# Kernel optimization log

Measured on AMD Instinct MI355X. Metric: run time of the kernel, lower is better.

The kernel has to match this reference:

```python
import jax, jax.numpy as jnp
import numpy as np

OUT = 3      # pooled output size (fmap_size//4 = 14//4 = 3)
RATIO = 2    # roi_align sampling ratio (fixed; torchvision adaptive ratio for 14/3 bins is 2)
P = 20       # num_persons


def _bilinear(fm, y, x):
    # fm: [C,H,W]; y,x broadcastable coordinate grids. torchvision aligned=False semantics.
    C, H, W = fm.shape
    y, x = jnp.broadcast_arrays(y, x)
    valid = (y > -1.0) & (y < H) & (x > -1.0) & (x < W)
    y = jnp.clip(y, 0.0, H - 1.0)
    x = jnp.clip(x, 0.0, W - 1.0)
    y0 = jnp.floor(y).astype(jnp.int32)
    x0 = jnp.floor(x).astype(jnp.int32)
    y1 = jnp.minimum(y0 + 1, H - 1)
    x1 = jnp.minimum(x0 + 1, W - 1)
    ly = y - y0
    lx = x - x0
    hy = 1.0 - ly
    hx = 1.0 - lx
    v00 = fm[:, y0, x0]
    v01 = fm[:, y0, x1]
    v10 = fm[:, y1, x0]
    v11 = fm[:, y1, x1]
    val = hy * hx * v00 + hy * lx * v01 + ly * hx * v10 + ly * lx * v11
    return jnp.where(valid, val, 0.0)  # [C, ...]


def _roi_align_one(fm, box):
    # fm: [C,H,W], box: [4] = (x1,y1,x2,y2) in feature-map coords -> [C,OUT,OUT]
    x1, y1, x2, y2 = box
    bw = (x2 - x1) / OUT
    bh = (y2 - y1) / OUT
    off = (jnp.arange(OUT * RATIO, dtype=fm.dtype) + 0.5) / RATIO  # bin-unit offsets
    xs = x1 + off * bw
    ys = y1 + off * bh
    vals = _bilinear(fm, ys[:, None], xs[None, :])  # [C, OUT*RATIO, OUT*RATIO]
    C = fm.shape[0]
    return vals.reshape(C, OUT, RATIO, OUT, RATIO).mean(axis=(2, 4))


def setup_inputs() -> dict:
    key = jax.random.key(0)
    ks = jax.random.split(key, 8)
    B, N, NB, C, FS = 128, 8, 27, 1024, 14
    fmap = jax.random.normal(ks[0], (B, C, FS, FS), jnp.float32)
    # boxes in feature-map coordinates with x1<x2, y1<y2
    lo = jax.random.uniform(ks[1], (B, N, 2), jnp.float32) * 10.0
    ext = 2.0 + jax.random.uniform(ks[2], (B, N, 2), jnp.float32) * 4.0
    hi = jnp.minimum(lo + ext, float(FS))
    boxes = jnp.concatenate([lo, hi], axis=-1)  # [B,N,4] (x1,y1,x2,y2)
    # unique person ids per frame (scatter target indices)
    pids = jax.vmap(lambda k: jax.random.permutation(k, P)[:N])(jax.random.split(ks[3], B)).astype(jnp.int32)
    w1 = jax.random.normal(ks[4], (512, C), jnp.float32) * 0.02
    w2 = jax.random.normal(ks[5], (256, 512), jnp.float32) * 0.05
    fc1_w = jax.random.normal(ks[6], (1024, 256 * OUT * OUT), jnp.float32) * 0.02
    fc1_b = jnp.zeros((1024,), jnp.float32)
    fc2_w = jax.random.normal(ks[7], (27, 1024), jnp.float32) * 0.02
    fc2_b = jnp.zeros((27,), jnp.float32)
    return {"fmap": fmap, "boxes": boxes, "pids": pids, "w1": w1, "w2": w2,
            "fc1_w": fc1_w, "fc1_b": fc1_b, "fc2_w": fc2_w, "fc2_b": fc2_b}


def _forward(fmap, boxes, pids, w1, w2, fc1_w, fc1_b, fc2_w, fc2_b):
    B, N = boxes.shape[:2]
    # per-image, per-box ROI align: [B,N,C,3,3]
    roi = jax.vmap(jax.vmap(_roi_align_one, in_axes=(None, 0)), in_axes=(0, 0))(fmap, boxes)
    # behavior_conv: two bias-free 1x1 convs (no nonlinearity between)
    h = jnp.einsum('bnchw,oc->bnohw', roi, w1)
    h = jnp.einsum('bnchw,oc->bnohw', h, w2)  # [B,N,256,3,3]
    feat = h.reshape(B, N, -1)                # [B,N,2304]
    bidx = jnp.broadcast_to(jnp.arange(B)[:, None], (B, N))
    # scatter into behavior_tensor keyed by person id (unique pids per frame -> well-defined)
    bt = jnp.zeros((B, P, feat.shape[-1]), feat.dtype).at[bidx, pids].set(feat)
    mean_b = bt.mean(axis=0)                  # [P,2304] mean over batch
    cur = bt[bidx, pids]                      # [B,N,2304]
    diff = mean_b[pids] - cur
    # behavior_fc (dropout is identity at inference)
    h1 = jax.nn.relu(jnp.einsum('bnd,hd->bnh', diff, fc1_w) + fc1_b)
    return jnp.einsum('bnh,oh->bno', h1, fc2_w) + fc2_b  # [B,N,num_behaviors]


def reference(fmap, boxes, pids, w1, w2, fc1_w, fc1_b, fc2_w, fc2_b):
    # fmap is detached and roi_align runs under no_grad in the original
    return _forward(jax.lax.stop_gradient(fmap), jax.lax.stop_gradient(boxes), pids,
                    w1, w2, fc1_w, fc1_b, fc2_w, fc2_b)
```

## Files before the change

kernel.cpp:

```cpp
#include <hip/hip_runtime.h>
#include <hip/hip_bf16.h>
#include <cstddef>
#include <cstdint>

#define B_   128
#define N_   8
#define C_   1024
#define FS_  14
#define POS_ 196
#define P_   20
#define HWC_ 9
#define ROWS_ 9216
#define CMID_ 256
#define FEATD_ 2304
#define H1_  1024
#define O_   27

typedef __attribute__((ext_vector_type(8))) short bf16x8;
typedef __attribute__((ext_vector_type(4))) float f32x4;

__device__ __forceinline__ void gld16(const void* g, void* l) {
    __builtin_amdgcn_global_load_lds(
        (const __attribute__((address_space(1))) unsigned int*)g,
        (__attribute__((address_space(3))) unsigned int*)l, 16, 0, 0);
}

__global__ __launch_bounds__(256) void wcombine_split_kernel(
    const float* __restrict__ w1,
    const float* __restrict__ w2,
    float* __restrict__ wpart)
{
    const int tid = threadIdx.x;
    const int tx = tid & 15, ty = tid >> 4;
    const int c0 = blockIdx.x * 64;
    const int o0 = blockIdx.y * 64;
    const int kb = blockIdx.z * 64;
    __shared__ __align__(16) float As[16][68];
    __shared__ __align__(16) float Bs[16][68];
    float acc[4][4] = {};
    for (int k0 = kb; k0 < kb + 64; k0 += 16) {
        for (int i = tid; i < 64 * 16; i += 256) {
            int k = i & 15, m = i >> 4;
            As[k][m] = w2[(size_t)(o0 + m) * 512 + k0 + k];
        }
        for (int i = tid; i < 64 * 16; i += 256) {
            int n = i & 63, k = i >> 6;
            Bs[k][n] = w1[(size_t)(k0 + k) * 1024 + c0 + n];
        }
        __syncthreads();
        #pragma unroll
        for (int k = 0; k < 16; ++k) {
            float4 a = *(const float4*)&As[k][ty * 4];
            float4 b = *(const float4*)&Bs[k][tx * 4];
            float av[4] = {a.x, a.y, a.z, a.w};
            float bv[4] = {b.x, b.y, b.z, b.w};
            #pragma unroll
            for (int i = 0; i < 4; ++i)
                #pragma unroll
                for (int j = 0; j < 4; ++j)
                    acc[i][j] += av[i] * bv[j];
        }
        __syncthreads();
    }
    float* dst = wpart + (size_t)blockIdx.z * (256 * 1024);
    for (int i = 0; i < 4; ++i) {
        float4 v = make_float4(acc[i][0], acc[i][1], acc[i][2], acc[i][3]);
        *(float4*)&dst[(size_t)(o0 + ty * 4 + i) * 1024 + c0 + tx * 4] = v;
    }
}

__global__ __launch_bounds__(256) void wc_reduce_kernel(
    const float* __restrict__ wpart, __hip_bfloat16* __restrict__ Wc)
{
    int idx = blockIdx.x * 256 + threadIdx.x;
    float s = 0.f;
    #pragma unroll
    for (int z = 0; z < 8; ++z) s += wpart[(size_t)z * (256 * 1024) + idx];
    Wc[idx] = __float2bfloat16(s);
}

__global__ __launch_bounds__(576) void roi_kernel(
    const float* __restrict__ fmap,
    const float* __restrict__ boxes,
    __hip_bfloat16* __restrict__ roi_mat)
{
    const int b = blockIdx.y;
    const int c0 = blockIdx.x * 64;
    const int tid = threadIdx.x;
    const int c_local = tid & 63;
    const int cell = tid >> 6;
    const int ch = cell / 3, cw = cell % 3;
    __shared__ float stage[64 * 197];

    const float* src = fmap + (size_t)(b * C_ + c0) * POS_;
    for (int i4 = tid; i4 < (64 * POS_) / 4; i4 += 576) {
        float4 v = ((const float4*)src)[i4];
        int base = i4 * 4;
        int c = base / POS_;
        int pos = base - c * POS_;
        float* dst = &stage[c * 197 + pos];
        dst[0] = v.x; dst[1] = v.y; dst[2] = v.z; dst[3] = v.w;
    }
    __syncthreads();

    const float* ch_ptr = &stage[c_local * 197];
    for (int n = 0; n < N_; ++n) {
        const float* bx = boxes + (size_t)(b * N_ + n) * 4;
        float x1 = bx[0], y1 = bx[1], x2 = bx[2], y2 = bx[3];
        float bw = (x2 - x1) * (1.0f / 3.0f);
        float bh = (y2 - y1) * (1.0f / 3.0f);
        float acc = 0.0f;
        #pragma unroll
        for (int si = 0; si < 2; ++si) {
            float yy = y1 + ((float)(2 * ch + si) + 0.5f) * 0.5f * bh;
            #pragma unroll
            for (int sj = 0; sj < 2; ++sj) {
                float xx = x1 + ((float)(2 * cw + sj) + 0.5f) * 0.5f * bw;
                bool valid = (yy > -1.0f) && (yy < (float)FS_) &&
                             (xx > -1.0f) && (xx < (float)FS_);
                float y = fminf(fmaxf(yy, 0.0f), (float)(FS_ - 1));
                float x = fminf(fmaxf(xx, 0.0f), (float)(FS_ - 1));
                int y0 = (int)floorf(y);
                int x0 = (int)floorf(x);
                int y1i = min(y0 + 1, FS_ - 1);
                int x1i = min(x0 + 1, FS_ - 1);
                float ly = y - (float)y0, lx = x - (float)x0;
                float hy = 1.0f - ly,     hx = 1.0f - lx;
                float v00 = ch_ptr[y0 * FS_ + x0];
                float v01 = ch_ptr[y0 * FS_ + x1i];
                float v10 = ch_ptr[y1i * FS_ + x0];
                float v11 = ch_ptr[y1i * FS_ + x1i];
                float val = hy * hx * v00 + hy * lx * v01 +
                            ly * hx * v10 + ly * lx * v11;
                acc += valid ? val : 0.0f;
            }
        }
        roi_mat[(size_t)((b * N_ + n) * HWC_ + cell) * C_ + c0 + c_local] =
            __float2bfloat16(acc * 0.25f);
    }
}

template<int EPI>
__global__ __launch_bounds__(256) void mfma_gemm_kernel(
    const __hip_bfloat16* __restrict__ A,
    const __hip_bfloat16* __restrict__ Bm,
    const float* __restrict__ bias,
    float* __restrict__ C, int K)
{
    const int tid = threadIdx.x;
    const int wave = tid >> 6, lane = tid & 63;
    const int r0 = blockIdx.y * 64, n0 = blockIdx.x * 64;
    const int wm = (wave >> 1) * 32, wn = (wave & 1) * 32;
    const int m16 = lane & 15, quad = lane >> 4;
    __shared__ __align__(16) __hip_bfloat16 As[64 * 64];
    __shared__ __align__(16) __hip_bfloat16 Bs[64 * 64];

    f32x4 acc[2][2];
    #pragma unroll
    for (int i = 0; i < 2; ++i)
        #pragma unroll
        for (int j = 0; j < 2; ++j)
            acc[i][j] = (f32x4){0.f, 0.f, 0.f, 0.f};

    const int s0 = wave * 64 + lane;
    const int ms0 = s0 >> 3, cs0 = (s0 & 7) ^ (ms0 & 7);
    const int s1 = 256 + s0;
    const int ms1 = s1 >> 3, cs1 = (s1 & 7) ^ (ms1 & 7);
    const size_t rA0 = (size_t)(r0 + ms0) * K + cs0 * 8;
    const size_t rA1 = (size_t)(r0 + ms1) * K + cs1 * 8;
    const size_t rB0 = (size_t)(n0 + ms0) * K + cs0 * 8;
    const size_t rB1 = (size_t)(n0 + ms1) * K + cs1 * 8;

    for (int k0 = 0; k0 < K; k0 += 64) {
        gld16(A + rA0 + k0, &As[wave * 512]);
        gld16(Bm + rB0 + k0, &Bs[wave * 512]);
        gld16(A + rA1 + k0, &As[2048 + wave * 512]);
        gld16(Bm + rB1 + k0, &Bs[2048 + wave * 512]);
        __syncthreads();
        #pragma unroll
        for (int ks = 0; ks < 2; ++ks) {
            bf16x8 af[2], bfv[2];
            #pragma unroll
            for (int t = 0; t < 2; ++t) {
                int m = wm + t * 16 + m16;
                int cp = (ks * 4 + quad) ^ (m & 7);
                af[t] = *(const bf16x8*)&As[(m * 8 + cp) * 8];
                int n = wn + t * 16 + m16;
                int cq = (ks * 4 + quad) ^ (n & 7);
                bfv[t] = *(const bf16x8*)&Bs[(n * 8 + cq) * 8];
            }
            #pragma unroll
            for (int i = 0; i < 2; ++i)
                #pragma unroll
                for (int j = 0; j < 2; ++j)
                    acc[i][j] = __builtin_amdgcn_mfma_f32_16x16x32_bf16(
                        af[i], bfv[j], acc[i][j], 0, 0, 0);
        }
        __syncthreads();
    }

    #pragma unroll
    for (int i = 0; i < 2; ++i) {
        #pragma unroll
        for (int j = 0; j < 2; ++j) {
            int col = n0 + wn + j * 16 + m16;
            int rbase = r0 + wm + i * 16 + quad * 4;
            if (EPI == 0) {
                #pragma unroll
                for (int g = 0; g < 4; ++g) {
                    int r = rbase + g;
                    int bn = r / 9, hw = r - bn * 9;
                    C[(size_t)bn * FEATD_ + hw * 256 + col] = acc[i][j][g];
                }
            } else {
                float bv = bias[col];
                #pragma unroll
                for (int g = 0; g < 4; ++g) {
                    int r = rbase + g;
                    float v = acc[i][j][g] + bv;
                    C[(size_t)r * H1_ + col] = v > 0.f ? v : 0.f;
                }
            }
        }
    }
}

__global__ __launch_bounds__(256) void fc1w_perm_kernel(
    const float* __restrict__ src, __hip_bfloat16* __restrict__ dst)
{
    int h = blockIdx.y;
    int d2 = blockIdx.x * 256 + threadIdx.x;
    int hw = d2 >> 8, o = d2 & 255;
    dst[(size_t)h * FEATD_ + d2] =
        __float2bfloat16(src[(size_t)h * FEATD_ + o * HWC_ + hw]);
}

__global__ __launch_bounds__(64) void invmap_kernel(
    const int* __restrict__ pids, int* __restrict__ inv)
{
    int b = blockIdx.x;
    int p = threadIdx.x;
    if (p < P_) {
        int v = -1;
        for (int n = 0; n < N_; ++n)
            if (pids[b * N_ + n] == p) v = n;
        inv[b * P_ + p] = v;
    }
}

__global__ __launch_bounds__(256) void meanb_kernel(
    const float* __restrict__ feat, const int* __restrict__ inv,
    float* __restrict__ mean_b)
{
    int p = blockIdx.x;
    int d = blockIdx.y * 256 + threadIdx.x;
    float acc = 0.0f;
    for (int b = 0; b < B_; ++b) {
        int n = inv[b * P_ + p];
        if (n >= 0) acc += feat[(size_t)(b * N_ + n) * FEATD_ + d];
    }
    mean_b[(size_t)p * FEATD_ + d] = acc * (1.0f / (float)B_);
}

__global__ __launch_bounds__(256) void diff_kernel(
    const float* __restrict__ feat, const float* __restrict__ mean_b,
    const int* __restrict__ pids, __hip_bfloat16* __restrict__ diff)
{
    int r = blockIdx.x;
    int pid = pids[r];
    const float* fr = feat + (size_t)r * FEATD_;
    const float* mr = mean_b + (size_t)pid * FEATD_;
    __hip_bfloat16* dr = diff + (size_t)r * FEATD_;
    for (int d = threadIdx.x; d < FEATD_; d += 256)
        dr[d] = __float2bfloat16(mr[d] - fr[d]);
}

__global__ __launch_bounds__(256) void fc2_kernel(
    const float* __restrict__ h1, const float* __restrict__ fc2_w,
    const float* __restrict__ fc2_b, float* __restrict__ out)
{
    int bn = blockIdx.x;
    int tid = threadIdx.x;
    __shared__ __align__(16) float row[H1_];
    __shared__ float partial[32][8];
    ((float4*)row)[tid] = ((const float4*)(h1 + (size_t)bn * H1_))[tid];
    __syncthreads();
    int o = tid >> 3, part = tid & 7;
    float acc = 0.0f;
    if (o < O_) {
        const float* wrow = fc2_w + (size_t)o * H1_ + part * 128;
        const float* hrow = row + part * 128;
        #pragma unroll 4
        for (int j = 0; j < 128; ++j) acc += hrow[j] * wrow[j];
    }
    partial[o][part] = acc;
    __syncthreads();
    if (part == 0 && o < O_) {
        float s = fc2_b[o];
        #pragma unroll
        for (int p = 0; p < 8; ++p) s += partial[o][p];
        out[(size_t)bn * O_ + o] = s;
    }
}

extern "C" void kernel_launch(void* const* d_in, const int* in_sizes, int n_in,
                              void* d_out, int out_size, void* d_ws, size_t ws_size,
                              hipStream_t stream) {
    const float* fmap  = (const float*)d_in[0];
    const float* boxes = (const float*)d_in[1];
    const int*   pids  = (const int*)  d_in[2];
    const float* w1    = (const float*)d_in[3];
    const float* w2    = (const float*)d_in[4];
    const float* fc1_w = (const float*)d_in[5];
    const float* fc1_b = (const float*)d_in[6];
    const float* fc2_w = (const float*)d_in[7];
    const float* fc2_b = (const float*)d_in[8];
    float* out = (float*)d_out;

    char* wsb = (char*)d_ws;
    __hip_bfloat16* Wc    = (__hip_bfloat16*)wsb;
    __hip_bfloat16* roi   = Wc + 256 * 1024;
    __hip_bfloat16* fc1wp = roi + (size_t)ROWS_ * C_;
    __hip_bfloat16* diffp = fc1wp + (size_t)H1_ * FEATD_;
    float* feat   = (float*)(diffp + (size_t)H1_ * FEATD_);
    float* mean_b = feat + (size_t)(B_ * N_) * FEATD_;
    float* h1     = mean_b + (size_t)P_ * FEATD_;
    int*   inv    = (int*)(h1 + (size_t)(B_ * N_) * H1_);
    float* wpart  = (float*)(inv + 128 * P_ + 64);

    hipLaunchKernelGGL(wcombine_split_kernel, dim3(16, 4, 8), dim3(256), 0, stream,
                       w1, w2, wpart);
    hipLaunchKernelGGL(wc_reduce_kernel, dim3(1024), dim3(256), 0, stream,
                       wpart, Wc);
    hipLaunchKernelGGL(roi_kernel, dim3(16, 128), dim3(576), 0, stream,
                       fmap, boxes, roi);
    hipLaunchKernelGGL(fc1w_perm_kernel, dim3(9, 1024), dim3(256), 0, stream,
                       fc1_w, fc1wp);
    hipLaunchKernelGGL((mfma_gemm_kernel<0>), dim3(4, 144), dim3(256), 0, stream,
                       roi, Wc, (const float*)nullptr, feat, 1024);
    hipLaunchKernelGGL(invmap_kernel, dim3(128), dim3(64), 0, stream,
                       pids, inv);
    hipLaunchKernelGGL(meanb_kernel, dim3(20, 9), dim3(256), 0, stream,
                       feat, inv, mean_b);
    hipLaunchKernelGGL(diff_kernel, dim3(1024), dim3(256), 0, stream,
                       feat, mean_b, pids, diffp);
    hipLaunchKernelGGL((mfma_gemm_kernel<1>), dim3(16, 16), dim3(256), 0, stream,
                       diffp, fc1wp, fc1_b, h1, FEATD_);
    hipLaunchKernelGGL(fc2_kernel, dim3(1024), dim3(256), 0, stream,
                       h1, fc2_w, fc2_b, out);
}
```

Measured before the change: 313.2 us.

## Apply channel-mixing GEMM before ROI align, on all feature-map positions

Since ROI align and the 1x1 convs are both linear, the combined weight is now applied to every fmap position (128*196 rows, K=1024, N=256) before ROI align. ROI align then samples the 256-channel bf16 result instead of 1024 fp32 channels and writes feat directly. This drops the 9216x1024 roi intermediate and cuts the bilinear work fourfold. In exchange the GEMM grows from 9216 to 25088 rows, and fmap is read with strided scalar loads and converted to bf16 inside the GEMM.

```diff
diff --git a/kernel.cpp b/kernel.cpp
--- a/kernel.cpp
+++ b/kernel.cpp
@@ -10,11 +10,11 @@
 #define POS_ 196
 #define P_   20
 #define HWC_ 9
-#define ROWS_ 9216
 #define CMID_ 256
 #define FEATD_ 2304
 #define H1_  1024
 #define O_   27
+#define GROWS_ (B_*POS_)
 
 typedef __attribute__((ext_vector_type(8))) short bf16x8;
 typedef __attribute__((ext_vector_type(4))) float f32x4;
@@ -79,31 +79,110 @@
     Wc[idx] = __float2bfloat16(s);
 }
 
-__global__ __launch_bounds__(576) void roi_kernel(
+__global__ __launch_bounds__(256, 3) void posgemm_kernel(
     const float* __restrict__ fmap,
+    const __hip_bfloat16* __restrict__ Wc,
+    __hip_bfloat16* __restrict__ G)
+{
+    const int tid = threadIdx.x;
+    const int wave = tid >> 6, lane = tid & 63;
+    const int m16 = lane & 15, quad = lane >> 4;
+    const int r0 = blockIdx.x * 64;
+
+    const int r = r0 + lane;
+    const int b_l = r / 196;
+    const int pos_l = r - b_l * 196;
+    const size_t abase = (size_t)b_l * (C_ * POS_) + pos_l;
+
+    __shared__ __align__(16) __hip_bfloat16 As[64 * 66];
+    __shared__ __align__(16) __hip_bfloat16 Bs[256 * 64];
+
+    f32x4 acc[4][4];
+    #pragma unroll
+    for (int i = 0; i < 4; ++i)
+        #pragma unroll
+        for (int j = 0; j < 4; ++j)
+            acc[i][j] = (f32x4){0.f, 0.f, 0.f, 0.f};
+
+    for (int k0 = 0; k0 < 1024; k0 += 64) {
+        #pragma unroll
+        for (int jj = 0; jj < 8; ++jj) {
+            int q = (wave * 8 + jj) * 64 + lane;
+            int mq = q >> 3, cq = q & 7;
+            int csq = cq ^ (mq & 7);
+            gld16(Wc + (size_t)mq * 1024 + k0 + csq * 8,
+                  (char*)Bs + (size_t)(wave * 8 + jj) * 1024);
+        }
+        #pragma unroll
+        for (int p = 0; p < 4; ++p) {
+            int cc = p * 16 + wave * 4;
+            const float* fp = fmap + abase + (size_t)(k0 + cc) * POS_;
+            float f0 = fp[0];
+            float f1 = fp[POS_];
+            float f2 = fp[2 * POS_];
+            float f3 = fp[3 * POS_];
+            __hip_bfloat162 q0, q1;
+            q0.x = __float2bfloat16(f0); q0.y = __float2bfloat16(f1);
+            q1.x = __float2bfloat16(f2); q1.y = __float2bfloat16(f3);
+            *(__hip_bfloat162*)&As[lane * 66 + cc]     = q0;
+            *(__hip_bfloat162*)&As[lane * 66 + cc + 2] = q1;
+        }
+        __syncthreads();
+        #pragma unroll
+        for (int ks = 0; ks < 2; ++ks) {
+            bf16x8 af[4], bfv[4];
+            #pragma unroll
+            for (int i = 0; i < 4; ++i) {
+                int m = i * 16 + m16;
+                af[i] = *(const bf16x8*)&As[m * 66 + (ks * 4 + quad) * 8];
+                int n = wave * 64 + i * 16 + m16;
+                int cq2 = (ks * 4 + quad) ^ (n & 7);
+                bfv[i] = *(const bf16x8*)&Bs[(n * 8 + cq2) * 8];
+            }
+            #pragma unroll
+            for (int i = 0; i < 4; ++i)
+                #pragma unroll
+                for (int j = 0; j < 4; ++j)
+                    acc[i][j] = __builtin_amdgcn_mfma_f32_16x16x32_bf16(
+                        af[i], bfv[j], acc[i][j], 0, 0, 0);
+        }
+        __syncthreads();
+    }
+
+    #pragma unroll
+    for (int i = 0; i < 4; ++i) {
+        #pragma unroll
+        for (int j = 0; j < 4; ++j) {
+            int col = wave * 64 + j * 16 + m16;
+            int rb = r0 + i * 16 + quad * 4;
+            #pragma unroll
+            for (int g = 0; g < 4; ++g)
+                G[(size_t)(rb + g) * 256 + col] = __float2bfloat16(acc[i][j][g]);
+        }
+    }
+}
+
+__global__ __launch_bounds__(576) void roi2_kernel(
+    const __hip_bfloat16* __restrict__ G,
     const float* __restrict__ boxes,
-    __hip_bfloat16* __restrict__ roi_mat)
+    float* __restrict__ feat)
 {
     const int b = blockIdx.y;
-    const int c0 = blockIdx.x * 64;
+    const int o0 = blockIdx.x * 64;
     const int tid = threadIdx.x;
-    const int c_local = tid & 63;
+    const int l = tid & 63;
     const int cell = tid >> 6;
     const int ch = cell / 3, cw = cell % 3;
-    __shared__ float stage[64 * 197];
-
-    const float* src = fmap + (size_t)(b * C_ + c0) * POS_;
-    for (int i4 = tid; i4 < (64 * POS_) / 4; i4 += 576) {
-        float4 v = ((const float4*)src)[i4];
-        int base = i4 * 4;
-        int c = base / POS_;
-        int pos = base - c * POS_;
-        float* dst = &stage[c * 197 + pos];
-        dst[0] = v.x; dst[1] = v.y; dst[2] = v.z; dst[3] = v.w;
+    __shared__ __align__(16) __hip_bfloat16 Ls[POS_ * 64];
+
+    for (int idx = tid; idx < POS_ * 8; idx += 576) {
+        int p = idx >> 3, chunk = idx & 7;
+        const uint4* src = (const uint4*)(G +
+            ((size_t)(b * POS_ + p) * 256 + o0 + chunk * 8));
+        *(uint4*)&Ls[p * 64 + chunk * 8] = *src;
     }
     __syncthreads();
 
-    const float* ch_ptr = &stage[c_local * 197];
     for (int n = 0; n < N_; ++n) {
         const float* bx = boxes + (size_t)(b * N_ + n) * 4;
         float x1 = bx[0], y1 = bx[1], x2 = bx[2], y2 = bx[3];
@@ -126,32 +205,31 @@
                 int x1i = min(x0 + 1, FS_ - 1);
                 float ly = y - (float)y0, lx = x - (float)x0;
                 float hy = 1.0f - ly,     hx = 1.0f - lx;
-                float v00 = ch_ptr[y0 * FS_ + x0];
-                float v01 = ch_ptr[y0 * FS_ + x1i];
-                float v10 = ch_ptr[y1i * FS_ + x0];
-                float v11 = ch_ptr[y1i * FS_ + x1i];
+                float v00 = __bfloat162float(Ls[(y0  * FS_ + x0 ) * 64 + l]);
+                float v01 = __bfloat162float(Ls[(y0  * FS_ + x1i) * 64 + l]);
+                float v10 = __bfloat162float(Ls[(y1i * FS_ + x0 ) * 64 + l]);
+                float v11 = __bfloat162float(Ls[(y1i * FS_ + x1i) * 64 + l]);
                 float val = hy * hx * v00 + hy * lx * v01 +
                             ly * hx * v10 + ly * lx * v11;
                 acc += valid ? val : 0.0f;
             }
         }
-        roi_mat[(size_t)((b * N_ + n) * HWC_ + cell) * C_ + c0 + c_local] =
-            __float2bfloat16(acc * 0.25f);
-    }
-}
-
-template<int EPI>
-__global__ __launch_bounds__(256) void mfma_gemm_kernel(
+        feat[(size_t)(b * N_ + n) * FEATD_ + cell * 256 + o0 + l] = acc * 0.25f;
+    }
+}
+
+__global__ __launch_bounds__(256) void fc1_gemm_kernel(
     const __hip_bfloat16* __restrict__ A,
     const __hip_bfloat16* __restrict__ Bm,
     const float* __restrict__ bias,
-    float* __restrict__ C, int K)
+    float* __restrict__ C)
 {
     const int tid = threadIdx.x;
     const int wave = tid >> 6, lane = tid & 63;
     const int r0 = blockIdx.y * 64, n0 = blockIdx.x * 64;
     const int wm = (wave >> 1) * 32, wn = (wave & 1) * 32;
     const int m16 = lane & 15, quad = lane >> 4;
+    const int K = FEATD_;
     __shared__ __align__(16) __hip_bfloat16 As[64 * 64];
     __shared__ __align__(16) __hip_bfloat16 Bs[64 * 64];
 
@@ -205,21 +283,12 @@
         for (int j = 0; j < 2; ++j) {
             int col = n0 + wn + j * 16 + m16;
             int rbase = r0 + wm + i * 16 + quad * 4;
-            if (EPI == 0) {
-                #pragma unroll
-                for (int g = 0; g < 4; ++g) {
-                    int r = rbase + g;
-                    int bn = r / 9, hw = r - bn * 9;
-                    C[(size_t)bn * FEATD_ + hw * 256 + col] = acc[i][j][g];
-                }
-            } else {
-                float bv = bias[col];
-                #pragma unroll
-                for (int g = 0; g < 4; ++g) {
-                    int r = rbase + g;
-                    float v = acc[i][j][g] + bv;
-                    C[(size_t)r * H1_ + col] = v > 0.f ? v : 0.f;
-                }
+            float bv = bias[col];
+            #pragma unroll
+            for (int g = 0; g < 4; ++g) {
+                int r = rbase + g;
+                float v = acc[i][j][g] + bv;
+                C[(size_t)r * H1_ + col] = v > 0.f ? v : 0.f;
             }
         }
     }
@@ -319,8 +388,8 @@
 
     char* wsb = (char*)d_ws;
     __hip_bfloat16* Wc    = (__hip_bfloat16*)wsb;
-    __hip_bfloat16* roi   = Wc + 256 * 1024;
-    __hip_bfloat16* fc1wp = roi + (size_t)ROWS_ * C_;
+    __hip_bfloat16* G     = Wc + 256 * 1024;
+    __hip_bfloat16* fc1wp = G + (size_t)GROWS_ * 256;
     __hip_bfloat16* diffp = fc1wp + (size_t)H1_ * FEATD_;
     float* feat   = (float*)(diffp + (size_t)H1_ * FEATD_);
     float* mean_b = feat + (size_t)(B_ * N_) * FEATD_;
@@ -332,20 +401,20 @@
                        w1, w2, wpart);
     hipLaunchKernelGGL(wc_reduce_kernel, dim3(1024), dim3(256), 0, stream,
                        wpart, Wc);
-    hipLaunchKernelGGL(roi_kernel, dim3(16, 128), dim3(576), 0, stream,
-                       fmap, boxes, roi);
+    hipLaunchKernelGGL(posgemm_kernel, dim3(GROWS_ / 64), dim3(256), 0, stream,
+                       fmap, Wc, G);
+    hipLaunchKernelGGL(roi2_kernel, dim3(4, 128), dim3(576), 0, stream,
+                       G, boxes, feat);
     hipLaunchKernelGGL(fc1w_perm_kernel, dim3(9, 1024), dim3(256), 0, stream,
                        fc1_w, fc1wp);
-    hipLaunchKernelGGL((mfma_gemm_kernel<0>), dim3(4, 144), dim3(256), 0, stream,
-                       roi, Wc, (const float*)nullptr, feat, 1024);
     hipLaunchKernelGGL(invmap_kernel, dim3(128), dim3(64), 0, stream,
                        pids, inv);
     hipLaunchKernelGGL(meanb_kernel, dim3(20, 9), dim3(256), 0, stream,
                        feat, inv, mean_b);
     hipLaunchKernelGGL(diff_kernel, dim3(1024), dim3(256), 0, stream,
                        feat, mean_b, pids, diffp);
-    hipLaunchKernelGGL((mfma_gemm_kernel<1>), dim3(16, 16), dim3(256), 0, stream,
-                       diffp, fc1wp, fc1_b, h1, FEATD_);
+    hipLaunchKernelGGL(fc1_gemm_kernel, dim3(16, 16), dim3(256), 0, stream,
+                       diffp, fc1wp, fc1_b, h1);
     hipLaunchKernelGGL(fc2_kernel, dim3(1024), dim3(256), 0, stream,
                        h1, fc2_w, fc2_b, out);
 }
```

Result: no change. 307.9 us (-1.7%).
